# Kernel optimization log

Measured on AMD Instinct MI355X. Metric: run time of the kernel, lower is better.

Reference implementation:

```python
import jax, jax.numpy as jnp
import numpy as np

N = 200000      # number of nodes / samples
D = 256         # embedding_dim
K = 20          # n_clusters


def setup_inputs() -> dict:
    key = jax.random.key(0)
    k1, k2 = jax.random.split(key)
    embeddings = jax.random.normal(k1, (N, D), dtype=jnp.float32)
    # indicator P has orthonormal-ish columns in the original (top-k eigenvectors
    # of ZZ^T); random values are fine for a correctness baseline of the math.
    indicator = jax.random.normal(k2, (N, K), dtype=jnp.float32)
    return {"embeddings": embeddings, "indicator": indicator}


def reference(embeddings, indicator):
    # Jc = tr(Z Z^T) - tr(P^T Z Z^T P)
    # tr(Z Z^T) = sum(Z * Z)
    term1 = jnp.sum(embeddings * embeddings)
    # tr(P^T Z Z^T P) = || Z^T P ||_F^2 ; Z^T P is [D, K] (tiny), avoids N x N gram.
    ztp = jnp.einsum('nd,nk->dk', embeddings, indicator)
    term2 = jnp.sum(ztp * ztp)
    return term1 - term2
```

## Files before the change

kernel.cpp:

```cpp
#include <hip/hip_runtime.h>

#define NN 200000
#define DD 256
#define KK 20
#define CHUNK 200
#define NB (NN / CHUNK)
#define NIT (CHUNK / 4)


#define SLOAD(i, zv) zv = Zr[(size_t)((((i) << 2) + w) * 64 + lane)];

#define SCOMP(i, zv)                                                        \
  {                                                                         \
    const float4* pr_ = (const float4*)(smem + ((((i) << 2) + w) * KK));    \
    float4 p0_ = pr_[0], p1_ = pr_[1], p2_ = pr_[2], p3_ = pr_[3],          \
           p4_ = pr_[4];                                                    \
    float zz_[4] = {zv.x, zv.y, zv.z, zv.w};                                \
    float pv_[KK] = {p0_.x, p0_.y, p0_.z, p0_.w, p1_.x, p1_.y, p1_.z,       \
                     p1_.w, p2_.x, p2_.y, p2_.z, p2_.w, p3_.x, p3_.y,       \
                     p3_.z, p3_.w, p4_.x, p4_.y, p4_.z, p4_.w};             \
    t1 += zz_[0] * zz_[0] + zz_[1] * zz_[1];                                \
    t1 += zz_[2] * zz_[2] + zz_[3] * zz_[3];                                \
    _Pragma("unroll") for (int k_ = 0; k_ < KK; ++k_) {                     \
      _Pragma("unroll") for (int c_ = 0; c_ < 4; ++c_)                      \
          acc[k_][c_] += zz_[c_] * pv_[k_];                                 \
    }                                                                       \
  }

__global__ __launch_bounds__(256, 3) void egac_main(
    const float* __restrict__ Z, const float* __restrict__ P,
    float* __restrict__ ztp_part, float* __restrict__ t1_part) {
  const int t = threadIdx.x;
  const int lane = t & 63;
  const int w = t >> 6;
  const int b = blockIdx.x;
  const int base = b * CHUNK;

  __shared__ float smem[KK * DD];
  __shared__ float wsum[4];

  {
    const float4* Psrc = (const float4*)(P + (size_t)base * KK);
    float4* pl4 = (float4*)smem;
    const int n4 = CHUNK * KK / 4;
#pragma unroll
    for (int i = 0; i < 4; ++i) {
      int idx = t + i * 256;
      if (idx < n4) pl4[idx] = Psrc[idx];
    }
  }
  __syncthreads();

  float acc[KK][4];
#pragma unroll
  for (int k = 0; k < KK; ++k)
#pragma unroll
    for (int c = 0; c < 4; ++c) acc[k][c] = 0.f;
  float t1 = 0.f;

  const float4* Zr = (const float4*)(Z + (size_t)base * DD);

  float4 zb[8];
#pragma unroll
  for (int j = 0; j < 6; ++j) SLOAD(j, zb[j]);

  for (int m = 0; m < 5; ++m) {
    const int s0 = m * 8;
#pragma unroll
    for (int u = 0; u < 8; ++u) {
      SLOAD(s0 + u + 6, zb[(u + 6) & 7]);
      SCOMP(s0 + u, zb[u]);
    }
  }
#pragma unroll
  for (int u = 0; u < 4; ++u) {
    SLOAD(40 + u + 6, zb[(u + 6) & 7]);
    SCOMP(40 + u, zb[u]);
  }
#pragma unroll
  for (int u = 4; u < 10; ++u) { SCOMP(40 + u, zb[u & 7]); }

  __syncthreads();
  float(*red)[DD] = (float(*)[DD])smem;
  for (int ph = 0; ph < 4; ++ph) {
    if (w == ph) {
      if (ph == 0) {
#pragma unroll
        for (int k = 0; k < KK; ++k)
          ((float4*)&red[k][0])[lane] =
              make_float4(acc[k][0], acc[k][1], acc[k][2], acc[k][3]);
      } else {
#pragma unroll
        for (int k = 0; k < KK; ++k) {
          float4 r = ((float4*)&red[k][0])[lane];
          r.x += acc[k][0];
          r.y += acc[k][1];
          r.z += acc[k][2];
          r.w += acc[k][3];
          ((float4*)&red[k][0])[lane] = r;
        }
      }
    }
    __syncthreads();
  }

#pragma unroll
  for (int off = 32; off > 0; off >>= 1) t1 += __shfl_xor(t1, off, 64);
  if (lane == 0) wsum[w] = t1;
  __syncthreads();

  float4* dst = (float4*)(ztp_part + (size_t)b * (KK * DD));
  const float4* src = (const float4*)&red[0][0];
#pragma unroll
  for (int i = 0; i < (KK * DD) / (4 * 256); ++i)
    dst[i * 256 + t] = src[i * 256 + t];
  if (t == 0) t1_part[b] = wsum[0] + wsum[1] + wsum[2] + wsum[3];
}

__global__ __launch_bounds__(512) void egac_reduce(
    const float* __restrict__ ztp_part, const float* __restrict__ t1_part,
    float* __restrict__ out, int nb) {
  __shared__ float red[16][32];
  const int t = threadIdx.x;
  const int el = t & 31;
  const int ps = t >> 5;
  const int e = blockIdx.x * 32 + el;

  float s = 0.f;
  for (int p = ps; p < nb; p += 16) s += ztp_part[(size_t)p * (KK * DD) + e];
  red[ps][el] = s;
  __syncthreads();
  for (int sh = 8; sh >= 1; sh >>= 1) {
    if (ps < sh) red[ps][el] += red[ps + sh][el];
    __syncthreads();
  }
  if (t == 0) {
    float ssq = 0.f;
#pragma unroll
    for (int i = 0; i < 32; ++i) {
      float v = red[0][i];
      ssq += v * v;
    }
    atomicAdd(out, -ssq);
  }

  if (blockIdx.x == 0) {
    float v = 0.f;
    for (int i = t; i < nb; i += 512) v += t1_part[i];
#pragma unroll
    for (int off = 32; off > 0; off >>= 1) v += __shfl_xor(v, off, 64);
    __shared__ float w2[8];
    if ((t & 63) == 0) w2[t >> 6] = v;
    __syncthreads();
    if (t == 0) {
      float tt = 0.f;
#pragma unroll
      for (int i = 0; i < 8; ++i) tt += w2[i];
      atomicAdd(out, tt);
    }
  }
}

extern "C" void kernel_launch(void* const* d_in, const int* in_sizes, int n_in,
                              void* d_out, int out_size, void* d_ws,
                              size_t ws_size, hipStream_t stream) {
  const float* Z = (const float*)d_in[0];
  const float* P = (const float*)d_in[1];
  float* out = (float*)d_out;

  float* ztp_part = (float*)d_ws;
  float* t1_part = (float*)d_ws + (size_t)NB * KK * DD;

  hipMemsetAsync(d_out, 0, sizeof(float), stream);
  egac_main<<<NB, 256, 0, stream>>>(Z, P, ztp_part, t1_part);
  egac_reduce<<<160, 512, 0, stream>>>(ztp_part, t1_part, out, NB);
}
```

Baseline: 356.6 us.

## Stream Z rows through per-wave LDS ring via async global_load_lds DMA

Replaces the register-based software pipeline of float4 global loads with a per-wave 8-deep LDS ring buffer filled by global_load_lds direct-to-LDS transfers, gated by explicit vmcnt waits. The aim is to keep more Z bytes in flight without spending VGPRs on prefetch buffers, which frees registers for the 80-float accumulator. In exchange, LDS use per block grows by about 32KB, every row costs an extra LDS read, and correctness now depends on hand-placed waitcnt ordering.

```diff
diff --git a/kernel.cpp b/kernel.cpp
--- a/kernel.cpp
+++ b/kernel.cpp
@@ -5,14 +5,19 @@
 #define KK 20
 #define CHUNK 200
 #define NB (NN / CHUNK)
-#define NIT (CHUNK / 4)
+#define RPW (CHUNK / 4)
+#define DEPTH 8
 
 
-#define SLOAD(i, zv) zv = Zr[(size_t)((((i) << 2) + w) * 64 + lane)];
+typedef __attribute__((address_space(3))) unsigned int lds_uint;
+typedef const __attribute__((address_space(1))) unsigned int glb_uint;
+#define DMA(gp, lp) \
+  __builtin_amdgcn_global_load_lds((glb_uint*)(gp), (lds_uint*)(lp), 16, 0, 0)
+#define WAITVM(N) asm volatile("s_waitcnt vmcnt(" #N ")" ::: "memory")
 
 #define SCOMP(i, zv)                                                        \
   {                                                                         \
-    const float4* pr_ = (const float4*)(smem + ((((i) << 2) + w) * KK));    \
+    const float4* pr_ = (const float4*)(pl + (((i) * 4 + w) * KK));         \
     float4 p0_ = pr_[0], p1_ = pr_[1], p2_ = pr_[2], p3_ = pr_[3],          \
            p4_ = pr_[4];                                                    \
     float zz_[4] = {zv.x, zv.y, zv.z, zv.w};                                \
@@ -27,27 +32,31 @@
     }                                                                       \
   }
 
-__global__ __launch_bounds__(256, 3) void egac_main(
+#define TAIL(S, N)                                                          \
+  {                                                                         \
+    WAITVM(N);                                                              \
+    float4 z = ((const float4*)(myring + ((S) & (DEPTH - 1)) * DD))[lane];  \
+    SCOMP(S, z);                                                            \
+  }
+
+__global__ __launch_bounds__(256)
+__attribute__((amdgpu_waves_per_eu(3, 3))) void egac_main(
     const float* __restrict__ Z, const float* __restrict__ P,
     float* __restrict__ ztp_part, float* __restrict__ t1_part) {
+  __shared__ float ring[4 * DEPTH * DD];
+  __shared__ float pl[CHUNK * KK];
+  __shared__ float wsum[4];
+
   const int t = threadIdx.x;
   const int lane = t & 63;
   const int w = t >> 6;
   const int b = blockIdx.x;
   const int base = b * CHUNK;
 
-  __shared__ float smem[KK * DD];
-  __shared__ float wsum[4];
-
   {
-    const float4* Psrc = (const float4*)(P + (size_t)base * KK);
-    float4* pl4 = (float4*)smem;
-    const int n4 = CHUNK * KK / 4;
-#pragma unroll
-    for (int i = 0; i < 4; ++i) {
-      int idx = t + i * 256;
-      if (idx < n4) pl4[idx] = Psrc[idx];
-    }
+    const float4* Ps = (const float4*)(P + (size_t)base * KK);
+    float4* pd = (float4*)pl;
+    for (int i = t; i < CHUNK * KK / 4; i += 256) pd[i] = Ps[i];
   }
   __syncthreads();
 
@@ -58,30 +67,26 @@
     for (int c = 0; c < 4; ++c) acc[k][c] = 0.f;
   float t1 = 0.f;
 
-  const float4* Zr = (const float4*)(Z + (size_t)base * DD);
+  const float* Zblk = Z + (size_t)base * DD;
+  float* myring = ring + w * (DEPTH * DD);
 
-  float4 zb[8];
 #pragma unroll
-  for (int j = 0; j < 6; ++j) SLOAD(j, zb[j]);
+  for (int q = 0; q < DEPTH; ++q)
+    DMA(Zblk + (4 * q + w) * DD + lane * 4, myring + q * DD);
 
-  for (int m = 0; m < 5; ++m) {
-    const int s0 = m * 8;
-#pragma unroll
-    for (int u = 0; u < 8; ++u) {
-      SLOAD(s0 + u + 6, zb[(u + 6) & 7]);
-      SCOMP(s0 + u, zb[u]);
-    }
+  for (int s = 0; s < RPW - DEPTH; ++s) {
+    WAITVM(7);
+    float4 z = ((const float4*)(myring + (s & (DEPTH - 1)) * DD))[lane];
+    asm volatile("" ::: "memory");
+    DMA(Zblk + (4 * (s + DEPTH) + w) * DD + lane * 4,
+        myring + (s & (DEPTH - 1)) * DD);
+    SCOMP(s, z);
   }
-#pragma unroll
-  for (int u = 0; u < 4; ++u) {
-    SLOAD(40 + u + 6, zb[(u + 6) & 7]);
-    SCOMP(40 + u, zb[u]);
-  }
-#pragma unroll
-  for (int u = 4; u < 10; ++u) { SCOMP(40 + u, zb[u & 7]); }
+  TAIL(42, 7); TAIL(43, 6); TAIL(44, 5); TAIL(45, 4);
+  TAIL(46, 3); TAIL(47, 2); TAIL(48, 1); TAIL(49, 0);
 
   __syncthreads();
-  float(*red)[DD] = (float(*)[DD])smem;
+  float(*red)[DD] = (float(*)[DD])ring;
   for (int ph = 0; ph < 4; ++ph) {
     if (w == ph) {
       if (ph == 0) {
```

After: 364.1 us. 2.1% more time.
